# Kernel tuning notes

Hardware: AMD Instinct MI355X
Metric: run time of the kernel (lower is better)

The kernel has to match this reference:

```python
import jax, jax.numpy as jnp
import numpy as np

B, T, D, H, E = 16, 4096, 256, 512, 8


def setup_inputs() -> dict:
    key = jax.random.key(0)
    ks = jax.random.split(key, 5)
    x = jax.random.normal(ks[0], (B, T, D), dtype=jnp.float32)
    gate_w = jax.random.normal(ks[1], (D, E), dtype=jnp.float32) * 0.02
    gate_b = jnp.zeros((E,), dtype=jnp.float32)
    W1 = jax.random.normal(ks[2], (E, D, H), dtype=jnp.float32) * 0.02
    b1 = jnp.zeros((E, H), dtype=jnp.float32)
    W2 = jax.random.normal(ks[3], (E, H, D), dtype=jnp.float32) * 0.02
    b2 = jnp.zeros((E, D), dtype=jnp.float32)
    return {"x": x, "gate_w": gate_w, "gate_b": gate_b,
            "W1": W1, "b1": b1, "W2": W2, "b2": b2}


def reference(x, gate_w, gate_b, W1, b1, W2, b2):
    Bb, Tt, Dd = x.shape
    Ee = gate_w.shape[1]
    xf = x.reshape(-1, Dd)                       # [N, D]
    N = xf.shape[0]
    logits = xf @ gate_w + gate_b                # [N, E]
    probs = jax.nn.softmax(logits, axis=-1)
    top2_vals, top2_idx = jax.lax.top_k(probs, 2)  # [N, 2]
    # combine weights: w[n, e] = sum_k top2_vals[n,k] * (top2_idx[n,k]==e)
    cw = jnp.zeros((N, Ee), dtype=xf.dtype).at[
        jnp.arange(N)[:, None], top2_idx].add(top2_vals)  # [N, E]

    def step(acc, params):
        w1, bb1, w2, bb2, we = params            # per-expert slices
        h = jax.nn.gelu(xf @ w1 + bb1, approximate=False)  # [N, H]
        y = h @ w2 + bb2                          # [N, D]
        return acc + we[:, None] * y, None

    out, _ = jax.lax.scan(step, jnp.zeros_like(xf),
                          (W1, b1, W2, b2, cw.T))
    return out.reshape(Bb, Tt, Dd)
```

## Files before the change

kernel.cpp:

```cpp
#include <hip/hip_runtime.h>
#include <hip/hip_bf16.h>
#include <math.h>


#define N_TOK 65536
#define D_DIM 256
#define H_DIM 512
#define TILE_R 64
#define GRID_TILES 1088

typedef __bf16 bf16x8 __attribute__((ext_vector_type(8)));
typedef float f32x4 __attribute__((ext_vector_type(4)));

static __device__ __forceinline__ ushort f2bf(float f) {
    __hip_bfloat16 h = __float2bfloat16(f);
    ushort u;
    __builtin_memcpy(&u, &h, 2);
    return u;
}

static __device__ __forceinline__ float gelu(float v) {
    const float a = fabsf(v) * 0.70710678118654752f;
    const float t = __builtin_amdgcn_rcpf(fmaf(a, 0.47047f, 1.0f));
    const float p = t * fmaf(t, fmaf(t, 0.7478556f, -0.0958798f), 0.3480242f);
    const float er = fmaf(-p, __expf(-a * a), 1.0f);
    const float s = copysignf(er, v);
    return 0.5f * v * (1.0f + s);
}

__global__ __launch_bounds__(256) void prep(const float* __restrict__ x,
                                            const float* __restrict__ gate_w,
                                            const float* __restrict__ gate_b,
                                            const float* __restrict__ W1,
                                            const float* __restrict__ W2,
                                            ushort* __restrict__ xb,
                                            ushort* __restrict__ W1p,
                                            ushort* __restrict__ W2p,
                                            int* __restrict__ counts,
                                            int* __restrict__ pid_arr,
                                            float2* __restrict__ pw_arr) {
    __shared__ float gwsT[8 * 260];
    __shared__ int lc[64];

    const int bid = blockIdx.x;
    const int tid = threadIdx.x;

    if (bid >= 2048) {
        const int pid = bid - 2048;
        const int t = (pid & 511) * 256 + tid;
        const int l = t & 63;
        const int lo = l & 15, hi = l >> 4;
        ushort v[8];
        if (pid < 512) {
            const int kb = (t >> 6) & 7;
            const int nb = (t >> 9) & 31;
            const int e  = t >> 14;
            const int k0 = kb * 32 + hi * 8;
            const int n  = nb * 16 + lo;
            const float* src = W1 + (size_t)e * D_DIM * H_DIM + n;
            #pragma unroll
            for (int j = 0; j < 8; ++j)
                v[j] = f2bf(src[(size_t)(k0 + j) * H_DIM]);
            *(uint4*)(W1p + (size_t)t * 8) = *(const uint4*)v;
        } else {
            const int kb = (t >> 6) & 15;
            const int nb = (t >> 10) & 15;
            const int e  = t >> 14;
            const int k0 = kb * 32 + hi * 8;
            const int n  = nb * 16 + lo;
            const float* src = W2 + (size_t)e * H_DIM * D_DIM + n;
            #pragma unroll
            for (int j = 0; j < 8; ++j)
                v[j] = f2bf(src[(size_t)(k0 + j) * D_DIM]);
            *(uint4*)(W2p + (size_t)t * 8) = *(const uint4*)v;
        }
        return;
    }

    const size_t t0 = (size_t)bid * 32;
    for (int i = tid; i < 2048; i += 256) {
        const int d = i >> 3, e = i & 7;
        gwsT[e * 260 + d] = gate_w[i];
    }
    if (tid < 64) lc[tid] = 0;
    __syncthreads();

    const int m = tid >> 3, q = tid & 7;
    const float* xrow = x + (t0 + m) * D_DIM;
    ushort* xbrow = xb + (t0 + m) * D_DIM;

    double lg[8] = {0, 0, 0, 0, 0, 0, 0, 0};
    #pragma unroll
    for (int it = 0; it < 8; ++it) {
        const int d0 = it * 32 + q * 4;
        const float4 v = *(const float4*)(xrow + d0);
        ushort4 bv;
        bv.x = f2bf(v.x); bv.y = f2bf(v.y); bv.z = f2bf(v.z); bv.w = f2bf(v.w);
        *(ushort4*)(xbrow + d0) = bv;
        const float vv[4] = {v.x, v.y, v.z, v.w};
        #pragma unroll
        for (int j = 0; j < 4; ++j) {
            const double xv = (double)vv[j];
            #pragma unroll
            for (int e2 = 0; e2 < 8; ++e2)
                lg[e2] += xv * (double)gwsT[e2 * 260 + d0 + j];
        }
    }
    #pragma unroll
    for (int e2 = 0; e2 < 8; ++e2) {
        lg[e2] += __shfl_xor(lg[e2], 1, 64);
        lg[e2] += __shfl_xor(lg[e2], 2, 64);
        lg[e2] += __shfl_xor(lg[e2], 4, 64);
    }

    if (q == 0) {
        int e0 = 0, e1 = -1;
        #pragma unroll
        for (int e2 = 0; e2 < 8; ++e2) lg[e2] += (double)gate_b[e2];
        double b0 = -1e300, b1v = -1e300;
        #pragma unroll
        for (int e2 = 0; e2 < 8; ++e2)
            if (lg[e2] > b0) { b0 = lg[e2]; e0 = e2; }
        #pragma unroll
        for (int e2 = 0; e2 < 8; ++e2)
            if (e2 != e0 && lg[e2] > b1v) { b1v = lg[e2]; e1 = e2; }
        double s = 0;
        #pragma unroll
        for (int e2 = 0; e2 < 8; ++e2) s += exp(lg[e2] - b0);
        const float p0 = (float)(1.0 / s);
        const float p1 = (float)(exp(b1v - b0) / s);
        const int pid = e0 * 8 + e1;
        atomicAdd(&lc[pid], 1);
        const int tok = (int)t0 + m;
        pid_arr[tok] = pid;
        pw_arr[tok] = make_float2(p0, p1);
    }
    __syncthreads();
    if (tid < 64 && lc[tid]) atomicAdd(&counts[tid], lc[tid]);
}

__global__ __launch_bounds__(256) void scatter(const int* __restrict__ counts,
                                               const int* __restrict__ pid_arr,
                                               const float2* __restrict__ pw_arr,
                                               int* __restrict__ cursor,
                                               int* __restrict__ tok_list,
                                               float* __restrict__ w0l,
                                               float* __restrict__ w1l) {
    __shared__ int lcnt[64];
    __shared__ int lbase[64];
    const int tid = threadIdx.x;
    const int t = blockIdx.x * 256 + tid;
    if (tid < 64) lcnt[tid] = 0;
    __syncthreads();
    const int pid = pid_arr[t];
    const float2 pw = pw_arr[t];
    const int lpos = atomicAdd(&lcnt[pid], 1);
    __syncthreads();
    if (tid < 64) {
        int s = 0;
        for (int i = 0; i < tid; ++i) s += counts[i];
        const int mine = lcnt[tid];
        lbase[tid] = s + (mine ? atomicAdd(&cursor[tid], mine) : 0);
    }
    __syncthreads();
    const int pos = lbase[pid] + lpos;
    tok_list[pos] = t;
    w0l[pos] = pw.x;
    w1l[pos] = pw.y;
}

__global__ __launch_bounds__(512, 4) void moe_expert(const ushort* __restrict__ xb,
                                                     const ushort* __restrict__ W1p,
                                                     const ushort* __restrict__ W2p,
                                                     const float* __restrict__ b1,
                                                     const float* __restrict__ b2,
                                                     const int* __restrict__ counts,
                                                     const int* __restrict__ tok_list,
                                                     const float* __restrict__ w0l,
                                                     const float* __restrict__ w1l,
                                                     float* __restrict__ out) {
    __shared__ __align__(16) char Xs[TILE_R * 512];
    __shared__ __align__(16) char Hs[TILE_R * 512];
    __shared__ int   toks[TILE_R];
    __shared__ float wgt[2][TILE_R];

    int n = 0;
    for (int i = 0; i < 64; ++i) n += (counts[i] + 63) >> 6;
    const int qn = n >> 3, rn = n & 7;
    const int xc = blockIdx.x & 7, ix = blockIdx.x >> 3;
    if (ix >= qn + (xc < rn ? 1 : 0)) return;
    const int wg = xc * qn + min(xc, rn) + ix;

    int pid = -1, row0 = 0, nv = 0, gbase = 0;
    int st = 0, sc = 0;
    for (int i = 0; i < 64; ++i) {
        const int c = counts[i];
        const int nt = (c + 63) >> 6;
        if (pid < 0 && wg < st + nt) { pid = i; row0 = (wg - st) << 6; nv = min(TILE_R, c - row0); gbase = sc; }
        st += nt; sc += c;
    }
    const int ea = pid >> 3, eb = pid & 7;
    const int gidx = gbase + row0;

    const int tid = threadIdx.x;
    const int w = tid >> 6, l = tid & 63;
    const int lo = l & 15, hi = l >> 4;

    if (tid < TILE_R) {
        const bool vld = tid < nv;
        const int src = gidx + (vld ? tid : 0);
        toks[tid]   = tok_list[src];
        wgt[0][tid] = vld ? w0l[src] : 0.f;
        wgt[1][tid] = vld ? w1l[src] : 0.f;
    }

    {
        const int r = tid >> 3;
        const int tk = tok_list[gidx + min(r, nv - 1)];
        const char* src = (const char*)(xb + (size_t)tk * D_DIM) + (tid & 7) * 64;
        char* dst = Xs + r * 512;
        const int bo = (tid & 7) * 64, sw = (r & 7) << 4;
        #pragma unroll
        for (int c = 0; c < 4; ++c)
            *(uint4*)(dst + ((bo + c * 16) ^ sw)) = *(const uint4*)(src + c * 16);
    }
    __syncthreads();

    f32x4 acc2[4][2];
    #pragma unroll
    for (int mi = 0; mi < 4; ++mi)
        #pragma unroll
        for (int ni = 0; ni < 2; ++ni)
            acc2[mi][ni] = (f32x4){0.f, 0.f, 0.f, 0.f};

    #pragma unroll 1
    for (int phase = 0; phase < 4; ++phase) {
        const int ph = phase >> 1, ch = phase & 1;
        const int ew = ph ? eb : ea;

        const char* w1b = (const char*)W1p + (size_t)(ew * 32 + ch * 16 + w * 2) * 8192 + (size_t)l * 16;

        f32x4 acc1[2][4];
        #pragma unroll
        for (int nb = 0; nb < 2; ++nb)
            #pragma unroll
            for (int tb = 0; tb < 4; ++tb)
                acc1[nb][tb] = (f32x4){0.f, 0.f, 0.f, 0.f};

        bf16x8 wf[2][2];
        wf[0][0] = *(const bf16x8*)(w1b);
        wf[0][1] = *(const bf16x8*)(w1b + 8192);

        #pragma unroll
        for (int ks = 0; ks < 8; ++ks) {
            const int cb = ks & 1, nx = cb ^ 1;
            if (ks < 7) {
                wf[nx][0] = *(const bf16x8*)(w1b + (ks + 1) * 1024);
                wf[nx][1] = *(const bf16x8*)(w1b + 8192 + (ks + 1) * 1024);
            }
            #pragma unroll
            for (int tb = 0; tb < 4; ++tb) {
                const int slot = tb * 16 + lo;
                const bf16x8 xf = *(const bf16x8*)(Xs + slot * 512 +
                                  ((ks * 64 + hi * 16) ^ ((slot & 7) << 4)));
                __builtin_amdgcn_s_setprio(1);
                #pragma unroll
                for (int nb = 0; nb < 2; ++nb)
                    acc1[nb][tb] = __builtin_amdgcn_mfma_f32_16x16x32_bf16(wf[cb][nb], xf, acc1[nb][tb], 0, 0, 0);
                __builtin_amdgcn_s_setprio(0);
            }
        }

        #pragma unroll
        for (int nb = 0; nb < 2; ++nb) {
            const int hcE = (ch * 16 + w * 2 + nb) * 16 + hi * 4;
            const int hcH = (w * 2 + nb) * 16 + hi * 4;
            const float4 b1q = *(const float4*)(b1 + ew * H_DIM + hcE);
            #pragma unroll
            for (int tb = 0; tb < 4; ++tb) {
                const int slot = tb * 16 + lo;
                const float wt = wgt[ph][slot];
                ushort4 hv;
                hv.x = f2bf(gelu(acc1[nb][tb][0] + b1q.x) * wt);
                hv.y = f2bf(gelu(acc1[nb][tb][1] + b1q.y) * wt);
                hv.z = f2bf(gelu(acc1[nb][tb][2] + b1q.z) * wt);
                hv.w = f2bf(gelu(acc1[nb][tb][3] + b1q.w) * wt);
                *(ushort4*)(Hs + slot * 512 + ((hcH * 2) ^ ((slot & 7) << 4))) = hv;
            }
        }

        const char* w2b = (const char*)W2p + ((size_t)(ew * 16 + w * 2) * 16 + ch * 8) * 1024 + (size_t)l * 16;
        bf16x8 wf2[3][2];
        #pragma unroll
        for (int p = 0; p < 2; ++p) {
            wf2[p][0] = *(const bf16x8*)(w2b + p * 1024);
            wf2[p][1] = *(const bf16x8*)(w2b + 16384 + p * 1024);
        }
        __syncthreads();

        #pragma unroll
        for (int ks = 0; ks < 8; ++ks) {
            const int cb = ks % 3;
            if (ks < 6) {
                const int lb = (ks + 2) % 3;
                wf2[lb][0] = *(const bf16x8*)(w2b + (ks + 2) * 1024);
                wf2[lb][1] = *(const bf16x8*)(w2b + 16384 + (ks + 2) * 1024);
            }
            #pragma unroll
            for (int mi = 0; mi < 4; ++mi) {
                const int slot = mi * 16 + lo;
                const bf16x8 hf = *(const bf16x8*)(Hs + slot * 512 +
                                  ((ks * 64 + hi * 16) ^ ((slot & 7) << 4)));
                __builtin_amdgcn_s_setprio(1);
                #pragma unroll
                for (int ni = 0; ni < 2; ++ni)
                    acc2[mi][ni] = __builtin_amdgcn_mfma_f32_16x16x32_bf16(hf, wf2[cb][ni], acc2[mi][ni], 0, 0, 0);
                __builtin_amdgcn_s_setprio(0);
            }
        }
        if (phase < 3) __syncthreads();
    }

    #pragma unroll
    for (int ni = 0; ni < 2; ++ni) {
        const int col = w * 32 + ni * 16 + lo;
        const float b2a = b2[ea * D_DIM + col];
        const float b2b = b2[eb * D_DIM + col];
        #pragma unroll
        for (int mi = 0; mi < 4; ++mi) {
            #pragma unroll
            for (int rg = 0; rg < 4; ++rg) {
                const int r = mi * 16 + hi * 4 + rg;
                if (r < nv) {
                    const float v = acc2[mi][ni][rg] + wgt[0][r] * b2a + wgt[1][r] * b2b;
                    out[(size_t)toks[r] * D_DIM + col] = v;
                }
            }
        }
    }
}

extern "C" void kernel_launch(void* const* d_in, const int* in_sizes, int n_in,
                              void* d_out, int out_size, void* d_ws, size_t ws_size,
                              hipStream_t stream) {
    const float* x      = (const float*)d_in[0];
    const float* gate_w = (const float*)d_in[1];
    const float* gate_b = (const float*)d_in[2];
    const float* W1     = (const float*)d_in[3];
    const float* b1     = (const float*)d_in[4];
    const float* W2     = (const float*)d_in[5];
    const float* b2     = (const float*)d_in[6];
    float* out = (float*)d_out;

    char* ws = (char*)d_ws;
    ushort* xb      = (ushort*)(ws);
    ushort* W1p     = (ushort*)(ws + 33554432);
    ushort* W2p     = (ushort*)(ws + 35651584);
    int*    pid_arr = (int*)   (ws + 37748736);
    float2* pw_arr  = (float2*)(ws + 38010880);
    int*    tok_lst = (int*)   (ws + 38535168);
    float*  w0l     = (float*) (ws + 38797312);
    float*  w1l     = (float*) (ws + 39059456);
    int*    counts  = (int*)   (ws + 39321600);
    int*    cursor  = (int*)   (ws + 39321856);

    hipMemsetAsync(counts, 0, 512, stream);

    prep<<<dim3(3072), 256, 0, stream>>>(x, gate_w, gate_b, W1, W2,
                                         xb, W1p, W2p, counts, pid_arr, pw_arr);
    scatter<<<dim3(256), 256, 0, stream>>>(counts, pid_arr, pw_arr, cursor,
                                           tok_lst, w0l, w1l);
    moe_expert<<<dim3(GRID_TILES), 512, 0, stream>>>(xb, W1p, W2p, b1, b2, counts,
                                                     tok_lst, w0l, w1l, out);
}
```

Before: 179.4 us.

## Double-buffer hidden tile in eight smaller phases to drop trailing barrier

The fused MoE expert loop is split into eight phases of 128 hidden columns instead of four of 256. The hidden-activation shared buffer is double-buffered at half size each, so the end-of-phase __syncthreads is removed and each phase needs only one barrier. The goal is to cut barrier stalls and let the next phase's GEMM1 overlap other waves' GEMM2. In exchange there are more phases, fewer MFMAs per weight load in GEMM1, and shorter prefetch pipelines.

```diff
diff --git a/kernel.cpp b/kernel.cpp
--- a/kernel.cpp
+++ b/kernel.cpp
@@ -180,7 +180,7 @@
                                                      const float* __restrict__ w1l,
                                                      float* __restrict__ out) {
     __shared__ __align__(16) char Xs[TILE_R * 512];
-    __shared__ __align__(16) char Hs[TILE_R * 512];
+    __shared__ __align__(16) char Hs[2][TILE_R * 256];
     __shared__ int   toks[TILE_R];
     __shared__ float wgt[2][TILE_R];
 
@@ -234,74 +234,67 @@
             acc2[mi][ni] = (f32x4){0.f, 0.f, 0.f, 0.f};
 
     #pragma unroll 1
-    for (int phase = 0; phase < 4; ++phase) {
-        const int ph = phase >> 1, ch = phase & 1;
+    for (int p = 0; p < 8; ++p) {
+        const int ph = p >> 2, qh = p & 3;
         const int ew = ph ? eb : ea;
-
-        const char* w1b = (const char*)W1p + (size_t)(ew * 32 + ch * 16 + w * 2) * 8192 + (size_t)l * 16;
-
-        f32x4 acc1[2][4];
-        #pragma unroll
-        for (int nb = 0; nb < 2; ++nb)
-            #pragma unroll
-            for (int tb = 0; tb < 4; ++tb)
-                acc1[nb][tb] = (f32x4){0.f, 0.f, 0.f, 0.f};
-
-        bf16x8 wf[2][2];
-        wf[0][0] = *(const bf16x8*)(w1b);
-        wf[0][1] = *(const bf16x8*)(w1b + 8192);
+        char* HsW = Hs[p & 1];
+
+        const char* w1b = (const char*)W1p + (size_t)(ew * 32 + qh * 8 + w) * 8192 + (size_t)l * 16;
+
+        f32x4 acc1[4];
+        #pragma unroll
+        for (int tb = 0; tb < 4; ++tb)
+            acc1[tb] = (f32x4){0.f, 0.f, 0.f, 0.f};
+
+        bf16x8 wf[2];
+        wf[0] = *(const bf16x8*)(w1b);
 
         #pragma unroll
         for (int ks = 0; ks < 8; ++ks) {
-            const int cb = ks & 1, nx = cb ^ 1;
-            if (ks < 7) {
-                wf[nx][0] = *(const bf16x8*)(w1b + (ks + 1) * 1024);
-                wf[nx][1] = *(const bf16x8*)(w1b + 8192 + (ks + 1) * 1024);
-            }
+            const int cb = ks & 1;
+            if (ks < 7)
+                wf[cb ^ 1] = *(const bf16x8*)(w1b + (ks + 1) * 1024);
             #pragma unroll
             for (int tb = 0; tb < 4; ++tb) {
                 const int slot = tb * 16 + lo;
                 const bf16x8 xf = *(const bf16x8*)(Xs + slot * 512 +
                                   ((ks * 64 + hi * 16) ^ ((slot & 7) << 4)));
                 __builtin_amdgcn_s_setprio(1);
-                #pragma unroll
-                for (int nb = 0; nb < 2; ++nb)
-                    acc1[nb][tb] = __builtin_amdgcn_mfma_f32_16x16x32_bf16(wf[cb][nb], xf, acc1[nb][tb], 0, 0, 0);
+                acc1[tb] = __builtin_amdgcn_mfma_f32_16x16x32_bf16(wf[cb], xf, acc1[tb], 0, 0, 0);
                 __builtin_amdgcn_s_setprio(0);
             }
         }
 
-        #pragma unroll
-        for (int nb = 0; nb < 2; ++nb) {
-            const int hcE = (ch * 16 + w * 2 + nb) * 16 + hi * 4;
-            const int hcH = (w * 2 + nb) * 16 + hi * 4;
+        {
+            const int hcE = (qh * 8 + w) * 16 + hi * 4;
+            const int hb  = (w * 16 + hi * 4) * 2;
             const float4 b1q = *(const float4*)(b1 + ew * H_DIM + hcE);
             #pragma unroll
             for (int tb = 0; tb < 4; ++tb) {
                 const int slot = tb * 16 + lo;
                 const float wt = wgt[ph][slot];
                 ushort4 hv;
-                hv.x = f2bf(gelu(acc1[nb][tb][0] + b1q.x) * wt);
-                hv.y = f2bf(gelu(acc1[nb][tb][1] + b1q.y) * wt);
-                hv.z = f2bf(gelu(acc1[nb][tb][2] + b1q.z) * wt);
-                hv.w = f2bf(gelu(acc1[nb][tb][3] + b1q.w) * wt);
-                *(ushort4*)(Hs + slot * 512 + ((hcH * 2) ^ ((slot & 7) << 4))) = hv;
-            }
-        }
-
-        const char* w2b = (const char*)W2p + ((size_t)(ew * 16 + w * 2) * 16 + ch * 8) * 1024 + (size_t)l * 16;
+                hv.x = f2bf(gelu(acc1[tb][0] + b1q.x) * wt);
+                hv.y = f2bf(gelu(acc1[tb][1] + b1q.y) * wt);
+                hv.z = f2bf(gelu(acc1[tb][2] + b1q.z) * wt);
+                hv.w = f2bf(gelu(acc1[tb][3] + b1q.w) * wt);
+                *(ushort4*)(HsW + slot * 256 + (hb ^ ((slot & 7) << 4))) = hv;
+            }
+        }
+
+        const char* w2b = (const char*)W2p + ((size_t)(ew * 16 + w * 2) * 16 + qh * 4) * 1024 + (size_t)l * 16;
         bf16x8 wf2[3][2];
         #pragma unroll
-        for (int p = 0; p < 2; ++p) {
-            wf2[p][0] = *(const bf16x8*)(w2b + p * 1024);
-            wf2[p][1] = *(const bf16x8*)(w2b + 16384 + p * 1024);
+        for (int pp = 0; pp < 2; ++pp) {
+            wf2[pp][0] = *(const bf16x8*)(w2b + pp * 1024);
+            wf2[pp][1] = *(const bf16x8*)(w2b + 16384 + pp * 1024);
         }
         __syncthreads();
 
         #pragma unroll
-        for (int ks = 0; ks < 8; ++ks) {
+        for (int ks = 0; ks < 4; ++ks) {
             const int cb = ks % 3;
-            if (ks < 6) {
+            if (ks < 2) {
                 const int lb = (ks + 2) % 3;
                 wf2[lb][0] = *(const bf16x8*)(w2b + (ks + 2) * 1024);
                 wf2[lb][1] = *(const bf16x8*)(w2b + 16384 + (ks + 2) * 1024);
@@ -309,7 +302,7 @@
             #pragma unroll
             for (int mi = 0; mi < 4; ++mi) {
                 const int slot = mi * 16 + lo;
-                const bf16x8 hf = *(const bf16x8*)(Hs + slot * 512 +
+                const bf16x8 hf = *(const bf16x8*)(HsW + slot * 256 +
                                   ((ks * 64 + hi * 16) ^ ((slot & 7) << 4)));
                 __builtin_amdgcn_s_setprio(1);
                 #pragma unroll
@@ -318,7 +311,6 @@
                 __builtin_amdgcn_s_setprio(0);
             }
         }
-        if (phase < 3) __syncthreads();
     }
 
     #pragma unroll
```

New measurement: 197.4 us. +10.1%, slower.
